# Kernel tuning notes

Measured on AMD Instinct MI355X. Metric: run time of the kernel, lower is better.

## Reference

```python
import jax, jax.numpy as jnp
import numpy as np

N_NODES = 50000
N_EDGES = 800000
IN_DIM, HID_DIM, OUT_DIM, N_HEADS = 256, 256, 64, 4
ATT_DIM = OUT_DIM * 2 + 1  # 129


def setup_inputs() -> dict:
    key = jax.random.key(0)
    ks = jax.random.split(key, 8)
    s = 0.05
    return {
        "x": jax.random.normal(ks[0], (N_NODES, IN_DIM), dtype=jnp.float32),
        "idx": jax.random.randint(ks[1], (2, N_EDGES), 0, N_NODES, dtype=jnp.int32),
        "elem": jax.random.uniform(ks[2], (N_EDGES,), dtype=jnp.float32),
        "W1": jax.random.normal(ks[3], (N_HEADS, IN_DIM, HID_DIM), dtype=jnp.float32) * s,
        "b1": jnp.zeros((N_HEADS, HID_DIM), jnp.float32),
        "W2": jax.random.normal(ks[4], (N_HEADS, HID_DIM, OUT_DIM), dtype=jnp.float32) * s,
        "b2": jnp.zeros((N_HEADS, OUT_DIM), jnp.float32),
        "A1": jax.random.normal(ks[5], (N_HEADS, ATT_DIM, ATT_DIM), dtype=jnp.float32) * s,
        "ab1": jnp.zeros((N_HEADS, ATT_DIM), jnp.float32),
        "A2": jax.random.normal(ks[6], (N_HEADS, ATT_DIM, 1), dtype=jnp.float32) * s,
        "ab2": jnp.zeros((N_HEADS, 1), jnp.float32),
    }


def reference(x, idx, elem, W1, b1, W2, b2, A1, ab1, A2, ab2):
    row, col = idx[0], idx[1]
    n = x.shape[0]

    def head(w1, bb1, w2, bb2, a1, aab1, a2, aab2):
        # 2-layer node MLP: [N, in] -> [N, out]
        feats = jnp.maximum(x @ w1 + bb1, 0.0) @ w2 + bb2
        # gather edge endpoints + edge value -> [E, 2*out+1]
        x_cat = jnp.concatenate([feats[row], feats[col], elem[:, None]], axis=1)
        # 2-layer edge attention MLP -> scalar per edge
        hid = jnp.maximum(x_cat @ a1 + aab1, 0.0)
        e1 = (hid @ a2 + aab2)[:, 0]
        e1 = jax.nn.leaky_relu(e1, negative_slope=0.2)
        w = jnp.exp(e1 - jnp.max(e1))  # global-max-stabilized exp
        # spmm: scatter weighted neighbor features into rows
        pooled = jax.ops.segment_sum(w[:, None] * feats[col], row, num_segments=n)
        row_sum = jax.ops.segment_sum(w, row, num_segments=n) + 1e-10
        return pooled / row_sum[:, None]  # [N, out]

    h = jax.vmap(head)(W1, b1, W2, b2, A1, ab1, A2, ab2)  # [H, N, out]
    return jnp.transpose(h, (1, 0, 2)).reshape(n, -1)  # concat heads -> [N, H*out]
```

## Files before the change

### kernel.cpp

```cpp
#include <hip/hip_runtime.h>
#include <hip/hip_bf16.h>

#define NNODES 50000
#define NEDGES 800000
#define IN_DIM 256
#define HID_DIM 256
#define OUT_DIM 64
#define NHEADS 4
#define ATT_DIM 129
#define PDIM 128
#define PJROWS 144
#define MAXD 64

#define XS_LD 264
#define FS_LD 72

#define LOG2E 1.44269504088896340736f

typedef unsigned short u16;
typedef unsigned char u8;
typedef unsigned int u32;
typedef __attribute__((ext_vector_type(8))) short bf16x8;
typedef __attribute__((ext_vector_type(4))) float f32x4;
typedef __attribute__((ext_vector_type(2))) float f32x2;
typedef __attribute__((ext_vector_type(2))) _Float16 h16x2;
typedef __fp16 hh2 __attribute__((ext_vector_type(2)));

__device__ __forceinline__ u16 f2bf(float f) {
  union { __hip_bfloat16 b; u16 u; } v;
  v.b = __float2bfloat16(f);
  return v.u;
}
__device__ __forceinline__ float bf2f(u16 b) {
  return __uint_as_float(((u32)b) << 16);
}
__device__ __forceinline__ h16x2 u2h2(u32 u) {
  union { u32 u; h16x2 h; } v; v.u = u; return v.h;
}
__device__ __forceinline__ u32 h2u(h16x2 h) {
  union { h16x2 h; u32 u; } v; v.h = h; return v.u;
}
__device__ __forceinline__ h16x2 pkrtz(float a, float b) {
  return __builtin_bit_cast(h16x2, __builtin_amdgcn_cvt_pkrtz(a, b));
}
__device__ __forceinline__ u32 cvt_pk_bf16(float a, float b) {
  u32 r;
  asm("v_cvt_pk_bf16_f32 %0, %1, %2" : "=v"(r) : "v"(a), "v"(b));
  return r;
}

__device__ __forceinline__ float dpp_sum16(float x) {
  int v;
  v = __builtin_amdgcn_update_dpp(0, __float_as_int(x), 0xB1, 0xF, 0xF, true);
  x += __int_as_float(v);
  v = __builtin_amdgcn_update_dpp(0, __float_as_int(x), 0x4E, 0xF, 0xF, true);
  x += __int_as_float(v);
  v = __builtin_amdgcn_update_dpp(0, __float_as_int(x), 0x141, 0xF, 0xF, true);
  x += __int_as_float(v);
  v = __builtin_amdgcn_update_dpp(0, __float_as_int(x), 0x140, 0xF, 0xF, true);
  x += __int_as_float(v);
  return x;
}

__global__ __launch_bounds__(256) void prep_kernel(
    const float* __restrict__ x, const int* __restrict__ idx,
    const float* __restrict__ elem, const float* __restrict__ W1,
    const float* __restrict__ W2, const float* __restrict__ A1,
    const float* __restrict__ ab1, const float* __restrict__ A2,
    const float* __restrict__ ab2, u16* __restrict__ xb,
    u16* __restrict__ W1T, u16* __restrict__ W2T,
    u16* __restrict__ A1Tr, u16* __restrict__ A1Tc,
    uint4* __restrict__ thE, uint4* __restrict__ thA2, uint4* __restrict__ thB1,
    float4* __restrict__ th_tail, u32* __restrict__ cnt, u32* __restrict__ ce)
{
  int id = blockIdx.x * 256 + threadIdx.x;
  {
    float4 a = *(const float4*)(x + (size_t)id * 8);
    float4 b = *(const float4*)(x + (size_t)id * 8 + 4);
    ushort4 o0, o1;
    o0.x = f2bf(a.x); o0.y = f2bf(a.y); o0.z = f2bf(a.z); o0.w = f2bf(a.w);
    o1.x = f2bf(b.x); o1.y = f2bf(b.y); o1.z = f2bf(b.z); o1.w = f2bf(b.w);
    *(ushort4*)(xb + (size_t)id * 8) = o0;
    *(ushort4*)(xb + (size_t)id * 8 + 4) = o1;
  }
  if (id < NEDGES) {
    int r = idx[id];
    u32 p = atomicAdd(&cnt[r], 1u);
    if (p < MAXD)
      ce[r * MAXD + p] = ((u32)f2bf(elem[id]) << 16) | (u32)idx[NEDGES + id];
  }
  if (id < NHEADS * 256 * 256) {
    int h = id >> 16, j = (id >> 8) & 255, k = id & 255;
    W1T[id] = f2bf(W1[(size_t)h * 65536 + k * 256 + j]);
  }
  if (id < NHEADS * 64 * 256) {
    int h = id >> 14, d = (id >> 8) & 63, j = id & 255;
    W2T[id] = f2bf(W2[(size_t)h * 16384 + j * 64 + d]);
  }
  if (id < NHEADS * PJROWS * 64) {
    int h = id / (PJROWS * 64);
    int rem = id % (PJROWS * 64);
    int j = rem >> 6, d = rem & 63;
    A1Tr[id] = (j < ATT_DIM) ? f2bf(A1[(size_t)h * 16641 + d * ATT_DIM + j]) : (u16)0;
    A1Tc[id] = (j < ATT_DIM) ? f2bf(A1[(size_t)h * 16641 + (64 + d) * ATT_DIM + j]) : (u16)0;
  }
  if (id < NHEADS * 16) {
    int h = id >> 4, m = id & 15;
    const float* Erow = A1 + (size_t)h * 16641 + (size_t)128 * ATT_DIM;
    uint4 e, a, b;
    u32* ep = (u32*)&e; u32* ap = (u32*)&a; u32* bp = (u32*)&b;
#pragma unroll
    for (int p = 0; p < 4; ++p) {
      int j = m * 8 + 2 * p;
      ep[p] = h2u(pkrtz(Erow[j], Erow[j + 1]));
      ap[p] = h2u(pkrtz(A2[h * ATT_DIM + j] * LOG2E, A2[h * ATT_DIM + j + 1] * LOG2E));
      bp[p] = h2u(pkrtz(ab1[h * ATT_DIM + j], ab1[h * ATT_DIM + j + 1]));
    }
    thE[id] = e; thA2[id] = a; thB1[id] = b;
  }
  if (id < NHEADS) {
    const float* Erow = A1 + (size_t)id * 16641 + (size_t)128 * ATT_DIM;
    th_tail[id] = make_float4(Erow[128], ab1[id * ATT_DIM + 128],
                              A2[id * ATT_DIM + 128] * LOG2E, ab2[id] * LOG2E);
  }
}

__global__ __launch_bounds__(256) void mlp_mfma_kernel(
    const u16* __restrict__ xb, const u16* __restrict__ W1T,
    const float* __restrict__ b1, const u16* __restrict__ W2T,
    const float* __restrict__ b2, const u16* __restrict__ A1Tr,
    const u16* __restrict__ A1Tc, u8* __restrict__ PF,
    u8* __restrict__ Pr8, u16* __restrict__ Prt, u16* __restrict__ Pct)
{
  __shared__ u16 xs[64 * XS_LD];
  __shared__ u16 hs[64 * XS_LD];
  const int h = blockIdx.y;
  const int n0 = blockIdx.x * 64;
  const int t = threadIdx.x;
  const int wv = t >> 6;
  const int l = t & 63;
  const int lr = l & 15;
  const int lq = l >> 4;

#pragma unroll
  for (int q = 0; q < 8; ++q) {
    int fi = q * 256 + t;
    int row = fi >> 5, c8 = fi & 31;
    int n = n0 + row;
    uint4 v = make_uint4(0, 0, 0, 0);
    if (n < NNODES) v = *(const uint4*)(xb + (size_t)n * IN_DIM + c8 * 8);
    *(uint4*)&xs[row * XS_LD + c8 * 8] = v;
  }
  __syncthreads();

  f32x4 acc[4][4];
#pragma unroll
  for (int ji = 0; ji < 4; ++ji)
#pragma unroll
    for (int ni = 0; ni < 4; ++ni) acc[ji][ni] = f32x4{0.f, 0.f, 0.f, 0.f};

  const u16* W1b = W1T + ((size_t)h * 256 + wv * 64) * 256;
#pragma unroll
  for (int kk = 0; kk < 8; ++kk) {
    const int ko = kk * 32 + lq * 8;
    bf16x8 w[4], xv[4];
#pragma unroll
    for (int ji = 0; ji < 4; ++ji)
      w[ji] = *(const bf16x8*)(W1b + (size_t)(ji * 16 + lr) * 256 + ko);
#pragma unroll
    for (int ni = 0; ni < 4; ++ni)
      xv[ni] = *(const bf16x8*)&xs[(ni * 16 + lr) * XS_LD + ko];
#pragma unroll
    for (int ji = 0; ji < 4; ++ji)
#pragma unroll
      for (int ni = 0; ni < 4; ++ni)
        acc[ji][ni] = __builtin_amdgcn_mfma_f32_16x16x32_bf16(w[ji], xv[ni], acc[ji][ni], 0, 0, 0);
  }
#pragma unroll
  for (int ji = 0; ji < 4; ++ji) {
    float4 bv = *(const float4*)(b1 + h * HID_DIM + wv * 64 + ji * 16 + lq * 4);
#pragma unroll
    for (int ni = 0; ni < 4; ++ni) {
      f32x4 v = acc[ji][ni];
      u32 lo = cvt_pk_bf16(fmaxf(v[0] + bv.x, 0.f), fmaxf(v[1] + bv.y, 0.f));
      u32 hi = cvt_pk_bf16(fmaxf(v[2] + bv.z, 0.f), fmaxf(v[3] + bv.w, 0.f));
      *(uint2*)&hs[(ni * 16 + lr) * XS_LD + wv * 64 + ji * 16 + lq * 4] = make_uint2(lo, hi);
    }
  }
  __syncthreads();

  f32x4 acc2[4];
#pragma unroll
  for (int ni = 0; ni < 4; ++ni) acc2[ni] = f32x4{0.f, 0.f, 0.f, 0.f};
  const u16* W2b = W2T + ((size_t)h * 64 + wv * 16) * 256;
#pragma unroll
  for (int kk = 0; kk < 8; ++kk) {
    const int ko = kk * 32 + lq * 8;
    bf16x8 wd = *(const bf16x8*)(W2b + (size_t)lr * 256 + ko);
#pragma unroll
    for (int ni = 0; ni < 4; ++ni) {
      bf16x8 hv = *(const bf16x8*)&hs[(ni * 16 + lr) * XS_LD + ko];
      acc2[ni] = __builtin_amdgcn_mfma_f32_16x16x32_bf16(wd, hv, acc2[ni], 0, 0, 0);
    }
  }
  u16* fs = xs;
  {
    float4 bv = *(const float4*)(b2 + h * OUT_DIM + wv * 16 + lq * 4);
    const int d0 = wv * 16 + lq * 4;
#pragma unroll
    for (int ni = 0; ni < 4; ++ni) {
      f32x4 v = acc2[ni];
      u32 lo = cvt_pk_bf16(v[0] + bv.x, v[1] + bv.y);
      u32 hi = cvt_pk_bf16(v[2] + bv.z, v[3] + bv.w);
      *(uint2*)&fs[(ni * 16 + lr) * FS_LD + d0] = make_uint2(lo, hi);
      int n = n0 + ni * 16 + lr;
      if (n < NNODES)
        *(uint2*)(PF + (size_t)n * 1024 + h * 256 + 128 + d0 * 2) = make_uint2(lo, hi);
    }
  }
  __syncthreads();

  for (int c = wv; c < 18; c += 4) {
    const int rc = c / 9;
    const int nf = c % 9;
    const u16* Ab = (rc ? A1Tc : A1Tr) + ((size_t)h * PJROWS + nf * 16) * 64;
    f32x4 acc3[4];
#pragma unroll
    for (int ni = 0; ni < 4; ++ni) acc3[ni] = f32x4{0.f, 0.f, 0.f, 0.f};
#pragma unroll
    for (int kk = 0; kk < 2; ++kk) {
      const int ko = kk * 32 + lq * 8;
      bf16x8 aj = *(const bf16x8*)(Ab + (size_t)lr * 64 + ko);
#pragma unroll
      for (int ni = 0; ni < 4; ++ni) {
        bf16x8 fv = *(const bf16x8*)&fs[(ni * 16 + lr) * FS_LD + ko];
        acc3[ni] = __builtin_amdgcn_mfma_f32_16x16x32_bf16(aj, fv, acc3[ni], 0, 0, 0);
      }
    }
#pragma unroll
    for (int ni = 0; ni < 4; ++ni) {
      int n = n0 + ni * 16 + lr;
      if (n >= NNODES) continue;
      if (nf == 8) {
        if (lq == 0) {
          u16 vb = f2bf(acc3[ni][0]);
          if (rc == 0) Prt[(size_t)h * NNODES + n] = vb;
          else         Pct[(size_t)n * NHEADS + h] = vb;
        }
      } else {
        const int j0 = nf * 16 + lq * 4;
        f32x4 v = acc3[ni];
        u32 pk = __builtin_amdgcn_cvt_pk_fp8_f32(v[0], v[1], 0, false);
        pk = __builtin_amdgcn_cvt_pk_fp8_f32(v[2], v[3], pk, true);
        if (rc == 0) *(u32*)(Pr8 + ((size_t)h * NNODES + n) * PDIM + j0) = pk;
        else         *(u32*)(PF + (size_t)n * 1024 + h * 256 + j0) = pk;
      }
    }
  }
}

__global__ __launch_bounds__(256) void edge_csr_kernel(
    const u8* __restrict__ PF, const u8* __restrict__ Pr8,
    const u16* __restrict__ Prt, const u16* __restrict__ Pct,
    const u32* __restrict__ cnt, const u32* __restrict__ ce,
    const uint4* __restrict__ thE, const uint4* __restrict__ thA2,
    const uint4* __restrict__ thB1, const float4* __restrict__ th_tail,
    float* __restrict__ out)
{
  const int r = blockIdx.x;
  const int h = threadIdx.x >> 6;
  const int l = threadIdx.x & 63;
  const int g = l >> 4;
  const int m = l & 15;

  const int deg = min((int)cnt[r], MAXD);
  if (deg == 0) {
    if (g == 0)
      *(float4*)(out + (size_t)r * (NHEADS * OUT_DIM) + h * OUT_DIM + m * 4) =
          make_float4(0.f, 0.f, 0.f, 0.f);
    return;
  }

  h16x2 Ej2[4], a2v2[4], prb2[4];
  {
    uint4 Eu = thE[h * 16 + m], Au = thA2[h * 16 + m], Bu = thB1[h * 16 + m];
    uint2 pr8v = *(const uint2*)(Pr8 + ((size_t)h * NNODES + r) * PDIM + m * 8);
    const u32* ep = (const u32*)&Eu;
    const u32* ap = (const u32*)&Au;
    const u32* bp = (const u32*)&Bu;
    f32x2 q01 = __builtin_amdgcn_cvt_pk_f32_fp8((int)pr8v.x, false);
    f32x2 q23 = __builtin_amdgcn_cvt_pk_f32_fp8((int)pr8v.x, true);
    f32x2 q45 = __builtin_amdgcn_cvt_pk_f32_fp8((int)pr8v.y, false);
    f32x2 q67 = __builtin_amdgcn_cvt_pk_f32_fp8((int)pr8v.y, true);
    h16x2 prh[4] = {pkrtz(q01[0], q01[1]), pkrtz(q23[0], q23[1]),
                    pkrtz(q45[0], q45[1]), pkrtz(q67[0], q67[1])};
#pragma unroll
    for (int p = 0; p < 4; ++p) {
      Ej2[p]  = u2h2(ep[p]);
      a2v2[p] = u2h2(ap[p]);
      prb2[p] = prh[p] + u2h2(bp[p]);
    }
  }
  const float4 tl = th_tail[h];
  float Et = 0.f, prtb = 0.f, a2t = 0.f;
  if (m == 0) {
    Et = tl.x;
    prtb = bf2f(Prt[(size_t)h * NNODES + r]) + tl.y;
    a2t = tl.z;
  }
  const float ab2v = tl.w;
  const h16x2 zero2 = {(_Float16)0.f, (_Float16)0.f};
  const u8* PFh = PF + h * 256;

  const u32* cebase = ce + r * MAXD;

  float acc0 = 0.f, acc1 = 0.f, acc2a = 0.f, acc3a = 0.f, wsum = 0.f;

  u32 cv = cebase[min(g, deg - 1)];
  u32 coloff = (cv & 0xffffu) << 10;
  float el = __uint_as_float(cv & 0xffff0000u);
  uint2 pc = *(const uint2*)(PFh + coloff + m * 8);
  ushort4 f4 = *(const ushort4*)(PFh + coloff + 128 + m * 8);
  float pctv = (m == 0) ? bf2f(Pct[(coloff >> 8) + h]) : 0.f;

  for (int k0 = 0; k0 < deg; k0 += 4) {
    int e1 = k0 + 4 + g;
    u32 cvn = cebase[min(e1, deg - 1)];
    u32 coln = (cvn & 0xffffu) << 10;
    float eln = __uint_as_float(cvn & 0xffff0000u);
    uint2 pcn = *(const uint2*)(PFh + coln + m * 8);
    ushort4 f4n = *(const ushort4*)(PFh + coln + 128 + m * 8);
    float pctvn = (m == 0) ? bf2f(Pct[(coln >> 8) + h]) : 0.f;

    float tsum = fmaxf(fmaf(el, Et, prtb + pctv), 0.f) * a2t;

    f32x2 v01 = __builtin_amdgcn_cvt_pk_f32_fp8((int)pc.x, false);
    f32x2 v23 = __builtin_amdgcn_cvt_pk_f32_fp8((int)pc.x, true);
    f32x2 v45 = __builtin_amdgcn_cvt_pk_f32_fp8((int)pc.y, false);
    f32x2 v67 = __builtin_amdgcn_cvt_pk_f32_fp8((int)pc.y, true);
    h16x2 pch[4] = {pkrtz(v01[0], v01[1]), pkrtz(v23[0], v23[1]),
                    pkrtz(v45[0], v45[1]), pkrtz(v67[0], v67[1])};
    const h16x2 el2 = pkrtz(el, el);

#pragma unroll
    for (int p = 0; p < 4; ++p) {
      h16x2 s = prb2[p] + pch[p];
      s = __builtin_elementwise_fma(el2, Ej2[p], s);
      s = __builtin_elementwise_max(s, zero2);
      tsum = __builtin_amdgcn_fdot2(__builtin_bit_cast(hh2, s),
                                    __builtin_bit_cast(hh2, a2v2[p]), tsum, false);
    }

    tsum = dpp_sum16(tsum);

    float e1f = tsum + ab2v;
    e1f = fmaxf(e1f, 0.2f * e1f);
    float w = exp2f(e1f);
    w = (k0 + g < deg) ? w : 0.f;

    acc0  = fmaf(w, bf2f(f4.x), acc0);
    acc1  = fmaf(w, bf2f(f4.y), acc1);
    acc2a = fmaf(w, bf2f(f4.z), acc2a);
    acc3a = fmaf(w, bf2f(f4.w), acc3a);
    wsum += w;

    pc = pcn; f4 = f4n; el = eln; pctv = pctvn;
  }

#pragma unroll
  for (int sh = 16; sh <= 32; sh <<= 1) {
    acc0  += __shfl_xor(acc0, sh);
    acc1  += __shfl_xor(acc1, sh);
    acc2a += __shfl_xor(acc2a, sh);
    acc3a += __shfl_xor(acc3a, sh);
    wsum  += __shfl_xor(wsum, sh);
  }
  if (g == 0) {
    float inv = 1.0f / (wsum + 1e-10f);
    float4 o = make_float4(acc0 * inv, acc1 * inv, acc2a * inv, acc3a * inv);
    *(float4*)(out + (size_t)r * (NHEADS * OUT_DIM) + h * OUT_DIM + m * 4) = o;
  }
}

extern "C" void kernel_launch(void* const* d_in, const int* in_sizes, int n_in,
                              void* d_out, int out_size, void* d_ws, size_t ws_size,
                              hipStream_t stream) {
  const float* x    = (const float*)d_in[0];
  const int*   idx  = (const int*)d_in[1];
  const float* elem = (const float*)d_in[2];
  const float* W1   = (const float*)d_in[3];
  const float* b1   = (const float*)d_in[4];
  const float* W2   = (const float*)d_in[5];
  const float* b2   = (const float*)d_in[6];
  const float* A1   = (const float*)d_in[7];
  const float* ab1  = (const float*)d_in[8];
  const float* A2   = (const float*)d_in[9];
  const float* ab2  = (const float*)d_in[10];
  float* out = (float*)d_out;

  u16* xb  = (u16*)d_ws;
  u8*  Pr8 = (u8*)(xb + (size_t)NNODES * IN_DIM);
  u8*  PF  = Pr8 + (size_t)NHEADS * NNODES * PDIM;
  u16* Prt = (u16*)(PF + (size_t)NNODES * 1024);
  u16* Pct = Prt + (size_t)NHEADS * NNODES;
  u32* cnt = (u32*)(Pct + (size_t)NHEADS * NNODES);
  u32* ce  = cnt + NNODES;
  u16* W1T  = (u16*)(ce + (size_t)NNODES * MAXD);
  u16* W2T  = W1T + NHEADS * 256 * 256;
  u16* A1Tr = W2T + NHEADS * 64 * 256;
  u16* A1Tc = A1Tr + NHEADS * PJROWS * 64;
  uint4* thE  = (uint4*)(A1Tc + NHEADS * PJROWS * 64);
  uint4* thA2 = thE + NHEADS * 16;
  uint4* thB1 = thA2 + NHEADS * 16;
  float4* th_tail = (float4*)(thB1 + NHEADS * 16);

  (void)hipMemsetAsync(cnt, 0, (size_t)NNODES * sizeof(u32), stream);

  prep_kernel<<<NNODES * IN_DIM / 8 / 256, 256, 0, stream>>>(
      x, idx, elem, W1, W2, A1, ab1, A2, ab2, xb, W1T, W2T, A1Tr, A1Tc,
      thE, thA2, thB1, th_tail, cnt, ce);

  dim3 gridM((NNODES + 63) / 64, NHEADS);
  mlp_mfma_kernel<<<gridM, 256, 0, stream>>>(xb, W1T, b1, W2T, b2, A1Tr, A1Tc,
                                             PF, Pr8, Prt, Pct);

  edge_csr_kernel<<<NNODES, 256, 0, stream>>>(PF, Pr8, Prt, Pct, cnt, ce,
                                              thE, thA2, thB1, th_tail, out);
}
```

Before: 349.2 us.

## Fuse x bf16 conversion into MLP kernel, process two heads per block, drop edge prefetch

The separate fp32-to-bf16 conversion of x in the prep kernel is removed. The MLP kernel now reads fp32 x directly and converts it while staging into shared memory. Each MLP block handles two heads, so the converted x tile is reused across them, and the grid's head dimension drops from 4 to 2. The prep grid shrinks to the edge count, and the edge kernel's software prefetch of the next edge group is removed to simplify the loop, at the risk of exposing gather latency.

```diff
diff --git a/kernel.cpp b/kernel.cpp
--- a/kernel.cpp
+++ b/kernel.cpp
@@ -63,26 +63,16 @@
 }
 
 __global__ __launch_bounds__(256) void prep_kernel(
-    const float* __restrict__ x, const int* __restrict__ idx,
-    const float* __restrict__ elem, const float* __restrict__ W1,
-    const float* __restrict__ W2, const float* __restrict__ A1,
-    const float* __restrict__ ab1, const float* __restrict__ A2,
-    const float* __restrict__ ab2, u16* __restrict__ xb,
+    const int* __restrict__ idx, const float* __restrict__ elem,
+    const float* __restrict__ W1, const float* __restrict__ W2,
+    const float* __restrict__ A1, const float* __restrict__ ab1,
+    const float* __restrict__ A2, const float* __restrict__ ab2,
     u16* __restrict__ W1T, u16* __restrict__ W2T,
     u16* __restrict__ A1Tr, u16* __restrict__ A1Tc,
     uint4* __restrict__ thE, uint4* __restrict__ thA2, uint4* __restrict__ thB1,
     float4* __restrict__ th_tail, u32* __restrict__ cnt, u32* __restrict__ ce)
 {
   int id = blockIdx.x * 256 + threadIdx.x;
-  {
-    float4 a = *(const float4*)(x + (size_t)id * 8);
-    float4 b = *(const float4*)(x + (size_t)id * 8 + 4);
-    ushort4 o0, o1;
-    o0.x = f2bf(a.x); o0.y = f2bf(a.y); o0.z = f2bf(a.z); o0.w = f2bf(a.w);
-    o1.x = f2bf(b.x); o1.y = f2bf(b.y); o1.z = f2bf(b.z); o1.w = f2bf(b.w);
-    *(ushort4*)(xb + (size_t)id * 8) = o0;
-    *(ushort4*)(xb + (size_t)id * 8 + 4) = o1;
-  }
   if (id < NEDGES) {
     int r = idx[id];
     u32 p = atomicAdd(&cnt[r], 1u);
@@ -126,7 +116,7 @@
 }
 
 __global__ __launch_bounds__(256) void mlp_mfma_kernel(
-    const u16* __restrict__ xb, const u16* __restrict__ W1T,
+    const float* __restrict__ x, const u16* __restrict__ W1T,
     const float* __restrict__ b1, const u16* __restrict__ W2T,
     const float* __restrict__ b2, const u16* __restrict__ A1Tr,
     const u16* __restrict__ A1Tc, u8* __restrict__ PF,
@@ -134,7 +124,7 @@
 {
   __shared__ u16 xs[64 * XS_LD];
   __shared__ u16 hs[64 * XS_LD];
-  const int h = blockIdx.y;
+  __shared__ u16 fs[64 * FS_LD];
   const int n0 = blockIdx.x * 64;
   const int t = threadIdx.x;
   const int wv = t >> 6;
@@ -143,119 +133,125 @@
   const int lq = l >> 4;
 
 #pragma unroll
-  for (int q = 0; q < 8; ++q) {
+  for (int q = 0; q < 16; ++q) {
     int fi = q * 256 + t;
-    int row = fi >> 5, c8 = fi & 31;
+    int row = fi >> 6, c4 = fi & 63;
     int n = n0 + row;
-    uint4 v = make_uint4(0, 0, 0, 0);
-    if (n < NNODES) v = *(const uint4*)(xb + (size_t)n * IN_DIM + c8 * 8);
-    *(uint4*)&xs[row * XS_LD + c8 * 8] = v;
+    float4 v = make_float4(0.f, 0.f, 0.f, 0.f);
+    if (n < NNODES) v = *(const float4*)(x + (size_t)n * IN_DIM + c4 * 4);
+    ushort4 o;
+    o.x = f2bf(v.x); o.y = f2bf(v.y); o.z = f2bf(v.z); o.w = f2bf(v.w);
+    *(ushort4*)&xs[row * XS_LD + c4 * 4] = o;
   }
   __syncthreads();
 
-  f32x4 acc[4][4];
-#pragma unroll
-  for (int ji = 0; ji < 4; ++ji)
-#pragma unroll
-    for (int ni = 0; ni < 4; ++ni) acc[ji][ni] = f32x4{0.f, 0.f, 0.f, 0.f};
-
-  const u16* W1b = W1T + ((size_t)h * 256 + wv * 64) * 256;
-#pragma unroll
-  for (int kk = 0; kk < 8; ++kk) {
-    const int ko = kk * 32 + lq * 8;
-    bf16x8 w[4], xv[4];
+  for (int hi = 0; hi < 2; ++hi) {
+    const int h = (int)blockIdx.y + hi * 2;
+
+    f32x4 acc[4][4];
 #pragma unroll
     for (int ji = 0; ji < 4; ++ji)
-      w[ji] = *(const bf16x8*)(W1b + (size_t)(ji * 16 + lr) * 256 + ko);
-#pragma unroll
-    for (int ni = 0; ni < 4; ++ni)
-      xv[ni] = *(const bf16x8*)&xs[(ni * 16 + lr) * XS_LD + ko];
-#pragma unroll
-    for (int ji = 0; ji < 4; ++ji)
+#pragma unroll
+      for (int ni = 0; ni < 4; ++ni) acc[ji][ni] = f32x4{0.f, 0.f, 0.f, 0.f};
+
+    const u16* W1b = W1T + ((size_t)h * 256 + wv * 64) * 256;
+#pragma unroll
+    for (int kk = 0; kk < 8; ++kk) {
+      const int ko = kk * 32 + lq * 8;
+      bf16x8 w[4], xv[4];
+#pragma unroll
+      for (int ji = 0; ji < 4; ++ji)
+        w[ji] = *(const bf16x8*)(W1b + (size_t)(ji * 16 + lr) * 256 + ko);
 #pragma unroll
       for (int ni = 0; ni < 4; ++ni)
-        acc[ji][ni] = __builtin_amdgcn_mfma_f32_16x16x32_bf16(w[ji], xv[ni], acc[ji][ni], 0, 0, 0);
-  }
-#pragma unroll
-  for (int ji = 0; ji < 4; ++ji) {
-    float4 bv = *(const float4*)(b1 + h * HID_DIM + wv * 64 + ji * 16 + lq * 4);
-#pragma unroll
-    for (int ni = 0; ni < 4; ++ni) {
-      f32x4 v = acc[ji][ni];
-      u32 lo = cvt_pk_bf16(fmaxf(v[0] + bv.x, 0.f), fmaxf(v[1] + bv.y, 0.f));
-      u32 hi = cvt_pk_bf16(fmaxf(v[2] + bv.z, 0.f), fmaxf(v[3] + bv.w, 0.f));
-      *(uint2*)&hs[(ni * 16 + lr) * XS_LD + wv * 64 + ji * 16 + lq * 4] = make_uint2(lo, hi);
-    }
-  }
-  __syncthreads();
-
-  f32x4 acc2[4];
-#pragma unroll
-  for (int ni = 0; ni < 4; ++ni) acc2[ni] = f32x4{0.f, 0.f, 0.f, 0.f};
-  const u16* W2b = W2T + ((size_t)h * 64 + wv * 16) * 256;
-#pragma unroll
-  for (int kk = 0; kk < 8; ++kk) {
-    const int ko = kk * 32 + lq * 8;
-    bf16x8 wd = *(const bf16x8*)(W2b + (size_t)lr * 256 + ko);
-#pragma unroll
-    for (int ni = 0; ni < 4; ++ni) {
-      bf16x8 hv = *(const bf16x8*)&hs[(ni * 16 + lr) * XS_LD + ko];
-      acc2[ni] = __builtin_amdgcn_mfma_f32_16x16x32_bf16(wd, hv, acc2[ni], 0, 0, 0);
-    }
-  }
-  u16* fs = xs;
-  {
-    float4 bv = *(const float4*)(b2 + h * OUT_DIM + wv * 16 + lq * 4);
-    const int d0 = wv * 16 + lq * 4;
-#pragma unroll
-    for (int ni = 0; ni < 4; ++ni) {
-      f32x4 v = acc2[ni];
-      u32 lo = cvt_pk_bf16(v[0] + bv.x, v[1] + bv.y);
-      u32 hi = cvt_pk_bf16(v[2] + bv.z, v[3] + bv.w);
-      *(uint2*)&fs[(ni * 16 + lr) * FS_LD + d0] = make_uint2(lo, hi);
-      int n = n0 + ni * 16 + lr;
-      if (n < NNODES)
-        *(uint2*)(PF + (size_t)n * 1024 + h * 256 + 128 + d0 * 2) = make_uint2(lo, hi);
-    }
-  }
-  __syncthreads();
-
-  for (int c = wv; c < 18; c += 4) {
-    const int rc = c / 9;
-    const int nf = c % 9;
-    const u16* Ab = (rc ? A1Tc : A1Tr) + ((size_t)h * PJROWS + nf * 16) * 64;
-    f32x4 acc3[4];
-#pragma unroll
-    for (int ni = 0; ni < 4; ++ni) acc3[ni] = f32x4{0.f, 0.f, 0.f, 0.f};
-#pragma unroll
-    for (int kk = 0; kk < 2; ++kk) {
+        xv[ni] = *(const bf16x8*)&xs[(ni * 16 + lr) * XS_LD + ko];
+#pragma unroll
+      for (int ji = 0; ji < 4; ++ji)
+#pragma unroll
+        for (int ni = 0; ni < 4; ++ni)
+          acc[ji][ni] = __builtin_amdgcn_mfma_f32_16x16x32_bf16(w[ji], xv[ni], acc[ji][ni], 0, 0, 0);
+    }
+#pragma unroll
+    for (int ji = 0; ji < 4; ++ji) {
+      float4 bv = *(const float4*)(b1 + h * HID_DIM + wv * 64 + ji * 16 + lq * 4);
+#pragma unroll
+      for (int ni = 0; ni < 4; ++ni) {
+        f32x4 v = acc[ji][ni];
+        u32 lo = cvt_pk_bf16(fmaxf(v[0] + bv.x, 0.f), fmaxf(v[1] + bv.y, 0.f));
+        u32 hi2 = cvt_pk_bf16(fmaxf(v[2] + bv.z, 0.f), fmaxf(v[3] + bv.w, 0.f));
+        *(uint2*)&hs[(ni * 16 + lr) * XS_LD + wv * 64 + ji * 16 + lq * 4] = make_uint2(lo, hi2);
+      }
+    }
+    __syncthreads();
+
+    f32x4 acc2[4];
+#pragma unroll
+    for (int ni = 0; ni < 4; ++ni) acc2[ni] = f32x4{0.f, 0.f, 0.f, 0.f};
+    const u16* W2b = W2T + ((size_t)h * 64 + wv * 16) * 256;
+#pragma unroll
+    for (int kk = 0; kk < 8; ++kk) {
       const int ko = kk * 32 + lq * 8;
-      bf16x8 aj = *(const bf16x8*)(Ab + (size_t)lr * 64 + ko);
+      bf16x8 wd = *(const bf16x8*)(W2b + (size_t)lr * 256 + ko);
 #pragma unroll
       for (int ni = 0; ni < 4; ++ni) {
-        bf16x8 fv = *(const bf16x8*)&fs[(ni * 16 + lr) * FS_LD + ko];
-        acc3[ni] = __builtin_amdgcn_mfma_f32_16x16x32_bf16(aj, fv, acc3[ni], 0, 0, 0);
+        bf16x8 hv = *(const bf16x8*)&hs[(ni * 16 + lr) * XS_LD + ko];
+        acc2[ni] = __builtin_amdgcn_mfma_f32_16x16x32_bf16(wd, hv, acc2[ni], 0, 0, 0);
       }
     }
-#pragma unroll
-    for (int ni = 0; ni < 4; ++ni) {
-      int n = n0 + ni * 16 + lr;
-      if (n >= NNODES) continue;
-      if (nf == 8) {
-        if (lq == 0) {
-          u16 vb = f2bf(acc3[ni][0]);
-          if (rc == 0) Prt[(size_t)h * NNODES + n] = vb;
-          else         Pct[(size_t)n * NHEADS + h] = vb;
+    {
+      float4 bv = *(const float4*)(b2 + h * OUT_DIM + wv * 16 + lq * 4);
+      const int d0 = wv * 16 + lq * 4;
+#pragma unroll
+      for (int ni = 0; ni < 4; ++ni) {
+        f32x4 v = acc2[ni];
+        u32 lo = cvt_pk_bf16(v[0] + bv.x, v[1] + bv.y);
+        u32 hi2 = cvt_pk_bf16(v[2] + bv.z, v[3] + bv.w);
+        *(uint2*)&fs[(ni * 16 + lr) * FS_LD + d0] = make_uint2(lo, hi2);
+        int n = n0 + ni * 16 + lr;
+        if (n < NNODES)
+          *(uint2*)(PF + (size_t)n * 1024 + h * 256 + 128 + d0 * 2) = make_uint2(lo, hi2);
+      }
+    }
+    __syncthreads();
+
+    for (int c = wv; c < 18; c += 4) {
+      const int rc = c / 9;
+      const int nf = c % 9;
+      const u16* Ab = (rc ? A1Tc : A1Tr) + ((size_t)h * PJROWS + nf * 16) * 64;
+      f32x4 acc3[4];
+#pragma unroll
+      for (int ni = 0; ni < 4; ++ni) acc3[ni] = f32x4{0.f, 0.f, 0.f, 0.f};
+#pragma unroll
+      for (int kk = 0; kk < 2; ++kk) {
+        const int ko = kk * 32 + lq * 8;
+        bf16x8 aj = *(const bf16x8*)(Ab + (size_t)lr * 64 + ko);
+#pragma unroll
+        for (int ni = 0; ni < 4; ++ni) {
+          bf16x8 fv = *(const bf16x8*)&fs[(ni * 16 + lr) * FS_LD + ko];
+          acc3[ni] = __builtin_amdgcn_mfma_f32_16x16x32_bf16(aj, fv, acc3[ni], 0, 0, 0);
         }
-      } else {
-        const int j0 = nf * 16 + lq * 4;
-        f32x4 v = acc3[ni];
-        u32 pk = __builtin_amdgcn_cvt_pk_fp8_f32(v[0], v[1], 0, false);
-        pk = __builtin_amdgcn_cvt_pk_fp8_f32(v[2], v[3], pk, true);
-        if (rc == 0) *(u32*)(Pr8 + ((size_t)h * NNODES + n) * PDIM + j0) = pk;
-        else         *(u32*)(PF + (size_t)n * 1024 + h * 256 + j0) = pk;
       }
-    }
+#pragma unroll
+      for (int ni = 0; ni < 4; ++ni) {
+        int n = n0 + ni * 16 + lr;
+        if (n >= NNODES) continue;
+        if (nf == 8) {
+          if (lq == 0) {
+            u16 vb = f2bf(acc3[ni][0]);
+            if (rc == 0) Prt[(size_t)h * NNODES + n] = vb;
+            else         Pct[(size_t)n * NHEADS + h] = vb;
+          }
+        } else {
+          const int j0 = nf * 16 + lq * 4;
+          f32x4 v = acc3[ni];
+          u32 pk = __builtin_amdgcn_cvt_pk_fp8_f32(v[0], v[1], 0, false);
+          pk = __builtin_amdgcn_cvt_pk_fp8_f32(v[2], v[3], pk, true);
+          if (rc == 0) *(u32*)(Pr8 + ((size_t)h * NNODES + n) * PDIM + j0) = pk;
+          else         *(u32*)(PF + (size_t)n * 1024 + h * 256 + j0) = pk;
+        }
+      }
+    }
+    __syncthreads();
   }
 }
 
@@ -316,21 +312,15 @@
 
   float acc0 = 0.f, acc1 = 0.f, acc2a = 0.f, acc3a = 0.f, wsum = 0.f;
 
-  u32 cv = cebase[min(g, deg - 1)];
-  u32 coloff = (cv & 0xffffu) << 10;
-  float el = __uint_as_float(cv & 0xffff0000u);
-  uint2 pc = *(const uint2*)(PFh + coloff + m * 8);
-  ushort4 f4 = *(const ushort4*)(PFh + coloff + 128 + m * 8);
-  float pctv = (m == 0) ? bf2f(Pct[(coloff >> 8) + h]) : 0.f;
-
   for (int k0 = 0; k0 < deg; k0 += 4) {
-    int e1 = k0 + 4 + g;
-    u32 cvn = cebase[min(e1, deg - 1)];
-    u32 coln = (cvn & 0xffffu) << 10;
-    float eln = __uint_as_float(cvn & 0xffff0000u);
-    uint2 pcn = *(const uint2*)(PFh + coln + m * 8);
-    ushort4 f4n = *(const ushort4*)(PFh + coln + 128 + m * 8);
-    float pctvn = (m == 0) ? bf2f(Pct[(coln >> 8) + h]) : 0.f;
+    const int e0 = k0 + g;
+    u32 cv = cebase[(e0 < deg) ? e0 : (deg - 1)];
+    u32 coloff = (cv & 0xffffu) << 10;
+    float el = __uint_as_float(cv & 0xffff0000u);
+
+    uint2 pc = *(const uint2*)(PFh + coloff + m * 8);
+    ushort4 f4 = *(const ushort4*)(PFh + coloff + 128 + m * 8);
+    float pctv = (m == 0) ? bf2f(Pct[(coloff >> 8) + h]) : 0.f;
 
     float tsum = fmaxf(fmaf(el, Et, prtb + pctv), 0.f) * a2t;
 
@@ -356,15 +346,13 @@
     float e1f = tsum + ab2v;
     e1f = fmaxf(e1f, 0.2f * e1f);
     float w = exp2f(e1f);
-    w = (k0 + g < deg) ? w : 0.f;
+    w = (e0 < deg) ? w : 0.f;
 
     acc0  = fmaf(w, bf2f(f4.x), acc0);
     acc1  = fmaf(w, bf2f(f4.y), acc1);
     acc2a = fmaf(w, bf2f(f4.z), acc2a);
     acc3a = fmaf(w, bf2f(f4.w), acc3a);
     wsum += w;
-
-    pc = pcn; f4 = f4n; el = eln; pctv = pctvn;
   }
 
 #pragma unroll
@@ -398,8 +386,7 @@
   const float* ab2  = (const float*)d_in[10];
   float* out = (float*)d_out;
 
-  u16* xb  = (u16*)d_ws;
-  u8*  Pr8 = (u8*)(xb + (size_t)NNODES * IN_DIM);
+  u8*  Pr8 = (u8*)d_ws;
   u8*  PF  = Pr8 + (size_t)NHEADS * NNODES * PDIM;
   u16* Prt = (u16*)(PF + (size_t)NNODES * 1024);
   u16* Pct = Prt + (size_t)NHEADS * NNODES;
@@ -416,12 +403,12 @@
 
   (void)hipMemsetAsync(cnt, 0, (size_t)NNODES * sizeof(u32), stream);
 
-  prep_kernel<<<NNODES * IN_DIM / 8 / 256, 256, 0, stream>>>(
-      x, idx, elem, W1, W2, A1, ab1, A2, ab2, xb, W1T, W2T, A1Tr, A1Tc,
+  prep_kernel<<<(NEDGES + 255) / 256, 256, 0, stream>>>(
+      idx, elem, W1, W2, A1, ab1, A2, ab2, W1T, W2T, A1Tr, A1Tc,
       thE, thA2, thB1, th_tail, cnt, ce);
 
-  dim3 gridM((NNODES + 63) / 64, NHEADS);
-  mlp_mfma_kernel<<<gridM, 256, 0, stream>>>(xb, W1T, b1, W2T, b2, A1Tr, A1Tc,
+  dim3 gridM((NNODES + 63) / 64, 2);
+  mlp_mfma_kernel<<<gridM, 256, 0, stream>>>(x, W1T, b1, W2T, b2, A1Tr, A1Tc,
                                              PF, Pr8, Prt, Pct);
 
   edge_csr_kernel<<<NNODES, 256, 0, stream>>>(PF, Pr8, Prt, Pct, cnt, ce,
```

Measured after the change: 340.6 us. -2.5%, faster.
